# Optimization experiments

Measured on AMD Instinct MI355X. Metric: run time of the kernel, lower is better.

## Reference

```python
import jax, jax.numpy as jnp
import numpy as np

B, N, K = 4, 4096, 32
NIN, RANK, NOUT, HID = 64, 16, 128, 64
EPS = 1e-7


def _ln(x, g, b, eps=1e-5):
    mu = jnp.mean(x, axis=-1, keepdims=True)
    var = jnp.mean((x - mu) ** 2, axis=-1, keepdims=True)
    return (x - mu) * jax.lax.rsqrt(var + eps) * g + b


def _zm(a):
    c, s = jnp.cos(a), jnp.sin(a)
    z, o = jnp.zeros_like(a), jnp.ones_like(a)
    return jnp.stack([c, -s, z, s, c, z, z, z, o], -1).reshape(*a.shape, 3, 3)


def _ym(a):
    c, s = jnp.cos(a), jnp.sin(a)
    z, o = jnp.zeros_like(a), jnp.ones_like(a)
    return jnp.stack([c, z, s, z, o, z, -s, z, c], -1).reshape(*a.shape, 3, 3)


def _rifeat(points_r, points_s):
    # points_r: (B,N,K,3); points_s: (B,N,1,3)
    r_mean = jnp.mean(points_r, axis=-2, keepdims=True)
    l1 = r_mean - points_r
    l2 = points_r - points_s
    l3 = points_s - r_mean  # (B,N,1,3)
    l1n = jnp.linalg.norm(l1, axis=-1, keepdims=True)
    l2n = jnp.linalg.norm(l2, axis=-1, keepdims=True)
    l3n = jnp.linalg.norm(l3, axis=-1, keepdims=True)  # (B,N,1,1)
    theta1 = jnp.sum(l1 * l2, -1, keepdims=True) / (l1n * l2n + EPS)
    theta2 = jnp.sum(l2 * l3, -1, keepdims=True) / (l2n * l3n + EPS)
    theta3 = jnp.sum(l3 * l1, -1, keepdims=True) / (l3n * l1n + EPS)
    # spherical angles of eval point; torch code swaps channels [0,2] then negates
    az = jnp.arctan2(points_s[..., 1], points_s[..., 0])          # (B,N,1)
    pol = jnp.arccos(jnp.clip(points_s[..., 2] / jnp.linalg.norm(points_s, axis=-1), -1.0, 1.0))
    sx = jnp.stack([-points_s[..., 2], -pol, -az], -1)            # (B,N,1,3)
    m = (_zm(sx[..., 0]) @ _ym(sx[..., 1]) @ _zm(sx[..., 2]))[:, :, 0]  # (B,N,3,3)
    h = jnp.linalg.norm(points_r, axis=-1, keepdims=True)         # (B,N,K,1)
    r_s2 = points_r / h
    res = jnp.einsum('bnxy,bnky->bnkx', m, r_s2)
    txj = jnp.arccos(jnp.clip(res[..., 2:3], -1.0, 1.0)) / np.pi
    l3n_b = jnp.broadcast_to(l3n, l1n.shape)
    return jnp.concatenate([txj, h, l1n, l2n, l3n_b, theta1, theta2, theta3], -1)  # (B,N,K,8)


def setup_inputs() -> dict:
    key = jax.random.key(0)
    ks = jax.random.split(key, 12)
    rn = lambda k, shape, s=1.0: jax.random.normal(k, shape, jnp.float32) * s
    return {
        'feat_points': rn(ks[0], (B, N, K, 3)),
        'feat': rn(ks[1], (B, N, K, NIN)),
        'eval_points': rn(ks[2], (B, N, 3)),
        # kernel MLP: Linear(8->HID) + LN + ReLU + Linear(HID->RANK)
        'w1': rn(ks[3], (8, HID), 1.0 / np.sqrt(8.0)),
        'b1': rn(ks[4], (HID,), 0.02),
        'g1': jnp.ones((HID,), jnp.float32),
        'be1': jnp.zeros((HID,), jnp.float32),
        'w2': rn(ks[5], (HID, RANK), 1.0 / np.sqrt(HID)),
        'b2': rn(ks[6], (RANK,), 0.02),
        # outnet: Linear(RANK*NIN -> NOUT)
        'wo': rn(ks[7], (RANK * NIN, NOUT), 1.0 / np.sqrt(RANK * NIN)),
        'bwo': rn(ks[8], (NOUT,), 0.02),
        # final LayerNorm
        'gln': jnp.ones((NOUT,), jnp.float32),
        'bln': jnp.zeros((NOUT,), jnp.float32),
    }


def reference(feat_points, feat, eval_points, w1, b1, g1, be1, w2, b2, wo, bwo, gln, bln):
    points_s = eval_points[:, :, None, :]                 # (B,N,1,3)
    ri = _rifeat(feat_points, points_s)                   # (B,N,K,8)
    hdn = jax.nn.relu(_ln(ri @ w1 + b1, g1, be1))         # (B,N,K,HID)
    kern = hdn @ w2 + b2                                  # (B,N,K,RANK)
    contracted = jnp.einsum('bnkr,bnki->bnri', kern, feat)
    contracted = contracted.reshape(feat.shape[0], feat.shape[1], -1)  # (B,N,RANK*NIN)
    out = contracted @ wo + bwo                           # (B,N,NOUT)
    return _ln(out, gln, bln)
```

## Files before the change

kernel.cpp:

```cpp
#include <hip/hip_runtime.h>
#include <hip/hip_bf16.h>

#define KP    32
#define NIN_  64
#define RNK   16
#define NOUT_ 128
#define HID_  64
#define CDIM  1024
#define EPS_  1e-7f
#define LNEPS 1e-5f
#define NTOT  16384

using short8 = __attribute__((ext_vector_type(8))) short;
using f32x4  = __attribute__((ext_vector_type(4))) float;

#define GLD16(gsrc, ldst) __builtin_amdgcn_global_load_lds( \
    (const __attribute__((address_space(1))) void*)(gsrc),  \
    (__attribute__((address_space(3))) void*)(ldst), 16, 0, 0)

__device__ __forceinline__ unsigned short f2bf(float x) {
  unsigned u = __float_as_uint(x);
  return (unsigned short)((u + 0x7fffu + ((u >> 16) & 1u)) >> 16);
}

__global__ __launch_bounds__(256) void k0_woT(const float* __restrict__ wo,
                                              unsigned short* __restrict__ woT) {
  __shared__ unsigned short S[64][129];
  const int t = threadIdx.x;
  const int k0 = blockIdx.x * 64;
  #pragma unroll
  for (int i = 0; i < 32; ++i) {
    const int idx = i * 256 + t;
    const int k = idx >> 7, n = idx & 127;
    S[k][n] = f2bf(wo[(long)(k0 + k) * NOUT_ + n]);
  }
  __syncthreads();
  #pragma unroll
  for (int i = 0; i < 32; ++i) {
    const int idx = i * 256 + t;
    const int n = idx >> 6, k = idx & 63;
    woT[(long)n * CDIM + k0 + k] = S[k][n];
  }
}

__global__ __launch_bounds__(256) void k1_contract(
    const float* __restrict__ fp,
    const float* __restrict__ feat,
    const float* __restrict__ ep,
    const float* __restrict__ w1,
    const float* __restrict__ b1, const float* __restrict__ g1,
    const float* __restrict__ be1,
    const float* __restrict__ w2,
    const float* __restrict__ b2,
    unsigned short* __restrict__ A)
{
  __shared__ float w1T[64][8];
  __shared__ float w2S[64][16];
  __shared__ float b1S[64], g1S[64], beS[64], b2S[16];
  __shared__ __align__(16) float featW[4][KP * NIN_];
  __shared__ float kernS[4][KP][17];

  const int t = threadIdx.x;
  const int wv = t >> 6, lane = t & 63;
  const int hh = lane & 1, kk = lane >> 1;

  if (t < 64) {
    #pragma unroll
    for (int x = 0; x < 8; ++x) w1T[t][x] = w1[x * HID_ + t];
    b1S[t] = b1[t]; g1S[t] = g1[t]; beS[t] = be1[t];
  }
  reinterpret_cast<float4*>(&w2S[0][0])[t] = reinterpret_cast<const float4*>(w2)[t];
  if (t < 16) b2S[t] = b2[t];
  __syncthreads();

  #pragma unroll 1
  for (int pi = 0; pi < 4; ++pi) {
    const long pt = (long)blockIdx.x * 16 + wv * 4 + pi;

    __builtin_amdgcn_sched_barrier(0);
    {
      const float* fsrc = feat + pt * (KP * NIN_);
      float* fdst = &featW[wv][0];
      #pragma unroll
      for (int j = 0; j < 8; ++j)
        GLD16(fsrc + j * 256 + lane * 4, fdst + j * 256 + lane * 4);
    }

    const float* prp = fp + (pt * KP + kk) * 3;
    float prx = prp[0], pry = prp[1], prz = prp[2];
    const float* psp = ep + pt * 3;
    float psx = psp[0], psy = psp[1], psz = psp[2];

    float sx = prx, sy = pry, sz = prz;
    #pragma unroll
    for (int m = 2; m <= 32; m <<= 1) {
      sx += __shfl_xor(sx, m); sy += __shfl_xor(sy, m); sz += __shfl_xor(sz, m);
    }
    const float inv = 1.f / 32.f;
    const float mx = sx * inv, my = sy * inv, mz = sz * inv;

    const float l1x = mx - prx, l1y = my - pry, l1z = mz - prz;
    const float l2x = prx - psx, l2y = pry - psy, l2z = prz - psz;
    const float l3x = psx - mx, l3y = psy - my, l3z = psz - mz;
    const float l1n = sqrtf(l1x * l1x + l1y * l1y + l1z * l1z);
    const float l2n = sqrtf(l2x * l2x + l2y * l2y + l2z * l2z);
    const float l3n = sqrtf(l3x * l3x + l3y * l3y + l3z * l3z);
    const float th1 = (l1x * l2x + l1y * l2y + l1z * l2z) / (l1n * l2n + EPS_);
    const float th2 = (l2x * l3x + l2y * l3y + l2z * l3z) / (l2n * l3n + EPS_);
    const float th3 = (l3x * l1x + l3y * l1y + l3z * l1z) / (l3n * l1n + EPS_);
    const float hn  = sqrtf(prx * prx + pry * pry + prz * prz);
    const float psn = sqrtf(psx * psx + psy * psy + psz * psz);
    float c = (psx * prx + psy * pry + psz * prz) / (psn * hn);
    c = fminf(1.f, fmaxf(-1.f, c));
    const float ri0 = acosf(c) * 0.31830988618379067f;
    const float ri1 = hn,  ri2 = l1n, ri3 = l2n;
    const float ri4 = l3n, ri5 = th1, ri6 = th2, ri7 = th3;

    float vals[32];
    #pragma unroll
    for (int j = 0; j < 32; ++j) {
      const int h = hh * 32 + j;
      const float4 wa = *reinterpret_cast<const float4*>(&w1T[h][0]);
      const float4 wb = *reinterpret_cast<const float4*>(&w1T[h][4]);
      vals[j] = b1S[h]
        + ri0 * wa.x + ri1 * wa.y + ri2 * wa.z + ri3 * wa.w
        + ri4 * wb.x + ri5 * wb.y + ri6 * wb.z + ri7 * wb.w;
    }
    float s = 0.f;
    #pragma unroll
    for (int j = 0; j < 32; ++j) s += vals[j];
    s += __shfl_xor(s, 1);
    const float mu = s * (1.f / 64.f);
    float v2 = 0.f;
    #pragma unroll
    for (int j = 0; j < 32; ++j) { const float d = vals[j] - mu; v2 += d * d; }
    v2 += __shfl_xor(v2, 1);
    const float rstd = rsqrtf(v2 * (1.f / 64.f) + LNEPS);
    #pragma unroll
    for (int j = 0; j < 32; ++j) {
      const int h = hh * 32 + j;
      vals[j] = fmaxf((vals[j] - mu) * rstd * g1S[h] + beS[h], 0.f);
    }

    float kern[16];
    #pragma unroll
    for (int r = 0; r < 16; ++r) kern[r] = 0.f;
    #pragma unroll
    for (int j = 0; j < 32; ++j) {
      const int h = hh * 32 + j;
      const float hv = vals[j];
      #pragma unroll
      for (int rc = 0; rc < 4; ++rc) {
        const float4 wr = *reinterpret_cast<const float4*>(&w2S[h][rc * 4]);
        kern[rc * 4 + 0] += hv * wr.x;
        kern[rc * 4 + 1] += hv * wr.y;
        kern[rc * 4 + 2] += hv * wr.z;
        kern[rc * 4 + 3] += hv * wr.w;
      }
    }
    #pragma unroll
    for (int r = 0; r < 16; ++r) kern[r] += __shfl_xor(kern[r], 1);
    #pragma unroll
    for (int q = 0; q < 8; ++q)
      kernS[wv][kk][hh * 8 + q] = kern[hh * 8 + q] + b2S[hh * 8 + q];

    asm volatile("s_waitcnt vmcnt(0)" ::: "memory");
    __builtin_amdgcn_sched_barrier(0);
    const int rr = lane & 15, riq = lane >> 4;
    f32x4 a0 = {0.f,0.f,0.f,0.f}, a1 = a0, a2 = a0, a3 = a0;
    #pragma unroll 8
    for (int kq = 0; kq < 32; ++kq) {
      const float kv = kernS[wv][kq][rr];
      const float* fb = &featW[wv][kq * 64 + riq * 4];
      const f32x4 f0 = *reinterpret_cast<const f32x4*>(fb);
      const f32x4 f1 = *reinterpret_cast<const f32x4*>(fb + 16);
      const f32x4 f2 = *reinterpret_cast<const f32x4*>(fb + 32);
      const f32x4 f3 = *reinterpret_cast<const f32x4*>(fb + 48);
      a0 += kv * f0; a1 += kv * f1; a2 += kv * f2; a3 += kv * f3;
    }
    unsigned short* Ap = A + pt * CDIM + rr * 64 + riq * 4;
    *reinterpret_cast<ushort4*>(Ap +  0) = make_ushort4(f2bf(a0[0]), f2bf(a0[1]), f2bf(a0[2]), f2bf(a0[3]));
    *reinterpret_cast<ushort4*>(Ap + 16) = make_ushort4(f2bf(a1[0]), f2bf(a1[1]), f2bf(a1[2]), f2bf(a1[3]));
    *reinterpret_cast<ushort4*>(Ap + 32) = make_ushort4(f2bf(a2[0]), f2bf(a2[1]), f2bf(a2[2]), f2bf(a2[3]));
    *reinterpret_cast<ushort4*>(Ap + 48) = make_ushort4(f2bf(a3[0]), f2bf(a3[1]), f2bf(a3[2]), f2bf(a3[3]));
  }
}

__global__ __launch_bounds__(256) void k2_gemm_ln(
    const unsigned short* __restrict__ A,
    const unsigned short* __restrict__ woT,
    const float* __restrict__ bwo, const float* __restrict__ gln,
    const float* __restrict__ bln, float* __restrict__ out)
{
  __shared__ __align__(16) char smem[49152];
  unsigned short* AsB = reinterpret_cast<unsigned short*>(smem);
  unsigned short* BsB = reinterpret_cast<unsigned short*>(smem + 16384);
  float* Cs = reinterpret_cast<float*>(smem);

  const int t = threadIdx.x;
  const int w = t >> 6, l = t & 63;
  const int mw = w & 1, nw = w >> 1;
  const long row0 = (long)blockIdx.x * 64;

  f32x4 acc[2][4];
  #pragma unroll
  for (int mt = 0; mt < 2; ++mt)
    #pragma unroll
    for (int nt = 0; nt < 4; ++nt) acc[mt][nt] = (f32x4){0.f, 0.f, 0.f, 0.f};

  auto stage = [&](int buf, int k0) {
    unsigned short* Ad = AsB + buf * 4096;
    unsigned short* Bd = BsB + buf * 8192;
    #pragma unroll
    for (int i = 0; i < 2; ++i) {
      const int idx = t + 256 * i;
      const int row = idx >> 3, c = idx & 7;
      const int cs = c ^ (row & 7);
      GLD16(A + (row0 + row) * CDIM + k0 + cs * 8, Ad + idx * 8);
    }
    #pragma unroll
    for (int i = 0; i < 4; ++i) {
      const int idx = t + 256 * i;
      const int row = idx >> 3, c = idx & 7;
      const int cs = c ^ (row & 7);
      GLD16(woT + (long)row * CDIM + k0 + cs * 8, Bd + idx * 8);
    }
  };

  stage(0, 0);
  asm volatile("s_waitcnt vmcnt(0)" ::: "memory");
  __builtin_amdgcn_s_barrier();

  for (int c = 0; c < 16; ++c) {
    const int cur = c & 1;
    if (c < 15) stage(cur ^ 1, (c + 1) * 64);

    const unsigned short* Ab = AsB + cur * 4096;
    const unsigned short* Bb = BsB + cur * 8192;
    const int kg = l >> 4, m = l & 15;
    #pragma unroll
    for (int ks = 0; ks < 2; ++ks) {
      const int kc = ks * 4 + kg;
      short8 af[2], bfr[4];
      #pragma unroll
      for (int mt = 0; mt < 2; ++mt) {
        const int row = mw * 32 + mt * 16 + m;
        af[mt] = *reinterpret_cast<const short8*>(&Ab[row * 64 + ((kc ^ (row & 7)) << 3)]);
      }
      #pragma unroll
      for (int nt = 0; nt < 4; ++nt) {
        const int row = nw * 64 + nt * 16 + m;
        bfr[nt] = *reinterpret_cast<const short8*>(&Bb[row * 64 + ((kc ^ (row & 7)) << 3)]);
      }
      #pragma unroll
      for (int mt = 0; mt < 2; ++mt)
        #pragma unroll
        for (int nt = 0; nt < 4; ++nt)
          acc[mt][nt] = __builtin_amdgcn_mfma_f32_16x16x32_bf16(
              af[mt], bfr[nt], acc[mt][nt], 0, 0, 0);
    }
    asm volatile("s_waitcnt vmcnt(0)" ::: "memory");
    __builtin_amdgcn_s_barrier();
  }

  #pragma unroll
  for (int mt = 0; mt < 2; ++mt)
    #pragma unroll
    for (int nt = 0; nt < 4; ++nt)
      #pragma unroll
      for (int r = 0; r < 4; ++r) {
        const int row = mw * 32 + mt * 16 + (l >> 4) * 4 + r;
        const int col = nw * 64 + nt * 16 + (l & 15);
        Cs[row * 132 + col] = acc[mt][nt][r];
      }
  __syncthreads();

  {
    const int row = t >> 2, q = t & 3;
    float4 v[8];
    #pragma unroll
    for (int i = 0; i < 8; ++i) {
      const float4 cv = *reinterpret_cast<const float4*>(&Cs[row * 132 + q * 32 + i * 4]);
      const float4 bv = *reinterpret_cast<const float4*>(&bwo[q * 32 + i * 4]);
      v[i] = make_float4(cv.x + bv.x, cv.y + bv.y, cv.z + bv.z, cv.w + bv.w);
    }
    float s = 0.f;
    #pragma unroll
    for (int i = 0; i < 8; ++i) s += v[i].x + v[i].y + v[i].z + v[i].w;
    s += __shfl_xor(s, 1); s += __shfl_xor(s, 2);
    const float mu = s * (1.f / 128.f);
    float d2 = 0.f;
    #pragma unroll
    for (int i = 0; i < 8; ++i) {
      const float dx = v[i].x - mu, dy = v[i].y - mu, dz = v[i].z - mu, dw = v[i].w - mu;
      d2 += dx * dx + dy * dy + dz * dz + dw * dw;
    }
    d2 += __shfl_xor(d2, 1); d2 += __shfl_xor(d2, 2);
    const float rstd = rsqrtf(d2 * (1.f / 128.f) + LNEPS);
    float* op = out + (row0 + row) * NOUT_ + q * 32;
    #pragma unroll
    for (int i = 0; i < 8; ++i) {
      const float4 gv = *reinterpret_cast<const float4*>(&gln[q * 32 + i * 4]);
      const float4 bv = *reinterpret_cast<const float4*>(&bln[q * 32 + i * 4]);
      float4 o;
      o.x = (v[i].x - mu) * rstd * gv.x + bv.x;
      o.y = (v[i].y - mu) * rstd * gv.y + bv.y;
      o.z = (v[i].z - mu) * rstd * gv.z + bv.z;
      o.w = (v[i].w - mu) * rstd * gv.w + bv.w;
      *reinterpret_cast<float4*>(op + i * 4) = o;
    }
  }
}

extern "C" void kernel_launch(void* const* d_in, const int* in_sizes, int n_in,
                              void* d_out, int out_size, void* d_ws, size_t ws_size,
                              hipStream_t stream) {
  const float* fp   = (const float*)d_in[0];
  const float* feat = (const float*)d_in[1];
  const float* ep   = (const float*)d_in[2];
  const float* w1   = (const float*)d_in[3];
  const float* b1   = (const float*)d_in[4];
  const float* g1   = (const float*)d_in[5];
  const float* be1  = (const float*)d_in[6];
  const float* w2   = (const float*)d_in[7];
  const float* b2   = (const float*)d_in[8];
  const float* wo   = (const float*)d_in[9];
  const float* bwo  = (const float*)d_in[10];
  const float* gln  = (const float*)d_in[11];
  const float* bln  = (const float*)d_in[12];
  float* out = (float*)d_out;

  unsigned short* A   = (unsigned short*)d_ws;
  unsigned short* woT = (unsigned short*)((char*)d_ws + (48u << 20));

  k0_woT<<<16, 256, 0, stream>>>(wo, woT);
  k1_contract<<<1024, 256, 0, stream>>>(fp, feat, ep, w1, b1, g1, be1, w2, b2, A);
  k2_gemm_ln<<<NTOT / 64, 256, 0, stream>>>(A, woT, bwo, gln, bln, out);
}
```

Before: 295.5 us.

## Read feat directly in contract kernel and shrink GEMM tile to 16 rows

The contract kernel no longer stages feat into LDS through async global-to-LDS loads. Each wave now processes 2 points instead of 4 and reads feat straight from global memory, and the grid doubles to 2048 blocks. The GEMM+LayerNorm kernel moves from 64-row to 16-row tiles with 1024 blocks and less LDS per block, trading more total woT reloads for more parallelism. It also drops the overlap of the feat load with the MLP compute and adds redundant reads of the B operand across blocks.

```diff
diff --git a/kernel.cpp b/kernel.cpp
--- a/kernel.cpp
+++ b/kernel.cpp
@@ -57,7 +57,6 @@
   __shared__ float w1T[64][8];
   __shared__ float w2S[64][16];
   __shared__ float b1S[64], g1S[64], beS[64], b2S[16];
-  __shared__ __align__(16) float featW[4][KP * NIN_];
   __shared__ float kernS[4][KP][17];
 
   const int t = threadIdx.x;
@@ -74,22 +73,13 @@
   __syncthreads();
 
   #pragma unroll 1
-  for (int pi = 0; pi < 4; ++pi) {
-    const long pt = (long)blockIdx.x * 16 + wv * 4 + pi;
-
-    __builtin_amdgcn_sched_barrier(0);
-    {
-      const float* fsrc = feat + pt * (KP * NIN_);
-      float* fdst = &featW[wv][0];
-      #pragma unroll
-      for (int j = 0; j < 8; ++j)
-        GLD16(fsrc + j * 256 + lane * 4, fdst + j * 256 + lane * 4);
-    }
+  for (int pi = 0; pi < 2; ++pi) {
+    const long pt = (long)blockIdx.x * 8 + wv * 2 + pi;
 
     const float* prp = fp + (pt * KP + kk) * 3;
-    float prx = prp[0], pry = prp[1], prz = prp[2];
+    const float prx = prp[0], pry = prp[1], prz = prp[2];
     const float* psp = ep + pt * 3;
-    float psx = psp[0], psy = psp[1], psz = psp[2];
+    const float psx = psp[0], psy = psp[1], psz = psp[2];
 
     float sx = prx, sy = pry, sz = prz;
     #pragma unroll
@@ -164,14 +154,13 @@
     for (int q = 0; q < 8; ++q)
       kernS[wv][kk][hh * 8 + q] = kern[hh * 8 + q] + b2S[hh * 8 + q];
 
-    asm volatile("s_waitcnt vmcnt(0)" ::: "memory");
-    __builtin_amdgcn_sched_barrier(0);
     const int rr = lane & 15, riq = lane >> 4;
+    const float* fbase = feat + pt * (KP * NIN_) + riq * 4;
     f32x4 a0 = {0.f,0.f,0.f,0.f}, a1 = a0, a2 = a0, a3 = a0;
     #pragma unroll 8
     for (int kq = 0; kq < 32; ++kq) {
       const float kv = kernS[wv][kq][rr];
-      const float* fb = &featW[wv][kq * 64 + riq * 4];
+      const float* fb = fbase + kq * 64;
       const f32x4 f0 = *reinterpret_cast<const f32x4*>(fb);
       const f32x4 f1 = *reinterpret_cast<const f32x4*>(fb + 16);
       const f32x4 f2 = *reinterpret_cast<const f32x4*>(fb + 32);
@@ -192,32 +181,26 @@
     const float* __restrict__ bwo, const float* __restrict__ gln,
     const float* __restrict__ bln, float* __restrict__ out)
 {
-  __shared__ __align__(16) char smem[49152];
+  __shared__ __align__(16) char smem[36864];
   unsigned short* AsB = reinterpret_cast<unsigned short*>(smem);
-  unsigned short* BsB = reinterpret_cast<unsigned short*>(smem + 16384);
+  unsigned short* BsB = reinterpret_cast<unsigned short*>(smem + 4096);
   float* Cs = reinterpret_cast<float*>(smem);
 
   const int t = threadIdx.x;
   const int w = t >> 6, l = t & 63;
-  const int mw = w & 1, nw = w >> 1;
-  const long row0 = (long)blockIdx.x * 64;
-
-  f32x4 acc[2][4];
-  #pragma unroll
-  for (int mt = 0; mt < 2; ++mt)
-    #pragma unroll
-    for (int nt = 0; nt < 4; ++nt) acc[mt][nt] = (f32x4){0.f, 0.f, 0.f, 0.f};
+  const long row0 = (long)blockIdx.x * 16;
+
+  f32x4 acc[2];
+  acc[0] = (f32x4){0.f, 0.f, 0.f, 0.f};
+  acc[1] = (f32x4){0.f, 0.f, 0.f, 0.f};
 
   auto stage = [&](int buf, int k0) {
-    unsigned short* Ad = AsB + buf * 4096;
+    if (t < 128) {
+      const int row = t >> 3, c = t & 7;
+      const int cs = c ^ (row & 7);
+      GLD16(A + (row0 + row) * CDIM + k0 + cs * 8, AsB + buf * 1024 + t * 8);
+    }
     unsigned short* Bd = BsB + buf * 8192;
-    #pragma unroll
-    for (int i = 0; i < 2; ++i) {
-      const int idx = t + 256 * i;
-      const int row = idx >> 3, c = idx & 7;
-      const int cs = c ^ (row & 7);
-      GLD16(A + (row0 + row) * CDIM + k0 + cs * 8, Ad + idx * 8);
-    }
     #pragma unroll
     for (int i = 0; i < 4; ++i) {
       const int idx = t + 256 * i;
@@ -235,73 +218,61 @@
     const int cur = c & 1;
     if (c < 15) stage(cur ^ 1, (c + 1) * 64);
 
-    const unsigned short* Ab = AsB + cur * 4096;
+    const unsigned short* Ab = AsB + cur * 1024;
     const unsigned short* Bb = BsB + cur * 8192;
     const int kg = l >> 4, m = l & 15;
     #pragma unroll
     for (int ks = 0; ks < 2; ++ks) {
       const int kc = ks * 4 + kg;
-      short8 af[2], bfr[4];
+      const short8 af = *reinterpret_cast<const short8*>(&Ab[m * 64 + ((kc ^ (m & 7)) << 3)]);
       #pragma unroll
-      for (int mt = 0; mt < 2; ++mt) {
-        const int row = mw * 32 + mt * 16 + m;
-        af[mt] = *reinterpret_cast<const short8*>(&Ab[row * 64 + ((kc ^ (row & 7)) << 3)]);
+      for (int nt = 0; nt < 2; ++nt) {
+        const int row = w * 32 + nt * 16 + m;
+        const short8 bf = *reinterpret_cast<const short8*>(&Bb[row * 64 + ((kc ^ (row & 7)) << 3)]);
+        acc[nt] = __builtin_amdgcn_mfma_f32_16x16x32_bf16(af, bf, acc[nt], 0, 0, 0);
       }
-      #pragma unroll
-      for (int nt = 0; nt < 4; ++nt) {
-        const int row = nw * 64 + nt * 16 + m;
-        bfr[nt] = *reinterpret_cast<const short8*>(&Bb[row * 64 + ((kc ^ (row & 7)) << 3)]);
-      }
-      #pragma unroll
-      for (int mt = 0; mt < 2; ++mt)
-        #pragma unroll
-        for (int nt = 0; nt < 4; ++nt)
-          acc[mt][nt] = __builtin_amdgcn_mfma_f32_16x16x32_bf16(
-              af[mt], bfr[nt], acc[mt][nt], 0, 0, 0);
     }
     asm volatile("s_waitcnt vmcnt(0)" ::: "memory");
     __builtin_amdgcn_s_barrier();
   }
 
   #pragma unroll
-  for (int mt = 0; mt < 2; ++mt)
-    #pragma unroll
-    for (int nt = 0; nt < 4; ++nt)
-      #pragma unroll
-      for (int r = 0; r < 4; ++r) {
-        const int row = mw * 32 + mt * 16 + (l >> 4) * 4 + r;
-        const int col = nw * 64 + nt * 16 + (l & 15);
-        Cs[row * 132 + col] = acc[mt][nt][r];
-      }
+  for (int nt = 0; nt < 2; ++nt)
+    #pragma unroll
+    for (int r = 0; r < 4; ++r) {
+      const int row = (l >> 4) * 4 + r;
+      const int col = w * 32 + nt * 16 + (l & 15);
+      Cs[row * 132 + col] = acc[nt][r];
+    }
   __syncthreads();
 
   {
-    const int row = t >> 2, q = t & 3;
-    float4 v[8];
-    #pragma unroll
-    for (int i = 0; i < 8; ++i) {
-      const float4 cv = *reinterpret_cast<const float4*>(&Cs[row * 132 + q * 32 + i * 4]);
-      const float4 bv = *reinterpret_cast<const float4*>(&bwo[q * 32 + i * 4]);
+    const int row = t >> 4, q = t & 15;
+    float4 v[2];
+    #pragma unroll
+    for (int i = 0; i < 2; ++i) {
+      const float4 cv = *reinterpret_cast<const float4*>(&Cs[row * 132 + q * 8 + i * 4]);
+      const float4 bv = *reinterpret_cast<const float4*>(&bwo[q * 8 + i * 4]);
       v[i] = make_float4(cv.x + bv.x, cv.y + bv.y, cv.z + bv.z, cv.w + bv.w);
     }
-    float s = 0.f;
-    #pragma unroll
-    for (int i = 0; i < 8; ++i) s += v[i].x + v[i].y + v[i].z + v[i].w;
+    float s = v[0].x + v[0].y + v[0].z + v[0].w + v[1].x + v[1].y + v[1].z + v[1].w;
     s += __shfl_xor(s, 1); s += __shfl_xor(s, 2);
+    s += __shfl_xor(s, 4); s += __shfl_xor(s, 8);
     const float mu = s * (1.f / 128.f);
     float d2 = 0.f;
     #pragma unroll
-    for (int i = 0; i < 8; ++i) {
+    for (int i = 0; i < 2; ++i) {
       const float dx = v[i].x - mu, dy = v[i].y - mu, dz = v[i].z - mu, dw = v[i].w - mu;
       d2 += dx * dx + dy * dy + dz * dz + dw * dw;
     }
     d2 += __shfl_xor(d2, 1); d2 += __shfl_xor(d2, 2);
+    d2 += __shfl_xor(d2, 4); d2 += __shfl_xor(d2, 8);
     const float rstd = rsqrtf(d2 * (1.f / 128.f) + LNEPS);
-    float* op = out + (row0 + row) * NOUT_ + q * 32;
-    #pragma unroll
-    for (int i = 0; i < 8; ++i) {
-      const float4 gv = *reinterpret_cast<const float4*>(&gln[q * 32 + i * 4]);
-      const float4 bv = *reinterpret_cast<const float4*>(&bln[q * 32 + i * 4]);
+    float* op = out + (row0 + row) * NOUT_ + q * 8;
+    #pragma unroll
+    for (int i = 0; i < 2; ++i) {
+      const float4 gv = *reinterpret_cast<const float4*>(&gln[q * 8 + i * 4]);
+      const float4 bv = *reinterpret_cast<const float4*>(&bln[q * 8 + i * 4]);
       float4 o;
       o.x = (v[i].x - mu) * rstd * gv.x + bv.x;
       o.y = (v[i].y - mu) * rstd * gv.y + bv.y;
@@ -334,6 +305,6 @@
   unsigned short* woT = (unsigned short*)((char*)d_ws + (48u << 20));
 
   k0_woT<<<16, 256, 0, stream>>>(wo, woT);
-  k1_contract<<<1024, 256, 0, stream>>>(fp, feat, ep, w1, b1, g1, be1, w2, b2, A);
-  k2_gemm_ln<<<NTOT / 64, 256, 0, stream>>>(A, woT, bwo, gln, bln, out);
-}
+  k1_contract<<<2048, 256, 0, stream>>>(fp, feat, ep, w1, b1, g1, be1, w2, b2, A);
+  k2_gemm_ln<<<1024, 256, 0, stream>>>(A, woT, bwo, gln, bln, out);
+}
```

New measurement: 570.4 us. 1.93x slower.
